# Optimization experiments

Hardware: AMD Instinct MI355X
Metric: run time of the kernel (lower is better)

The kernel has to match this reference:

```python
import jax, jax.numpy as jnp
import numpy as np

D = 1024
H = 16
HD = D // H
DFF = 4 * D
B, L = 2, 2048
EPS = 1e-5


def setup_inputs() -> dict:
    key = jax.random.key(0)
    ks = jax.random.split(key, 12)
    s = lambda fan_in: 1.0 / np.sqrt(fan_in)
    inp = {
        "x": jax.random.normal(ks[0], (B, L, D), jnp.float32),
        "mask": jnp.ones((1, 1, L, L), jnp.bool_),
        "ln_g": jnp.ones((D,), jnp.float32),
        "ln_b": jnp.zeros((D,), jnp.float32),
        "qkv_w": jax.random.uniform(ks[1], (3 * D, D), jnp.float32, -s(D), s(D)),
        "qkv_b": jax.random.uniform(ks[2], (3 * D,), jnp.float32, -s(D), s(D)),
        "wo_w": jax.random.uniform(ks[3], (D, D), jnp.float32, -s(D), s(D)),
        "wo_b": jax.random.uniform(ks[4], (D,), jnp.float32, -s(D), s(D)),
        "m0_w": jax.random.uniform(ks[5], (DFF, D), jnp.float32, -s(D), s(D)),
        "m0_b": jax.random.uniform(ks[6], (DFF,), jnp.float32, -s(D), s(D)),
        "m1_w": jax.random.uniform(ks[7], (D, DFF), jnp.float32, -s(DFF), s(DFF)),
        "m1_b": jax.random.uniform(ks[8], (D,), jnp.float32, -s(DFF), s(DFF)),
    }
    return inp


def _layer_norm(x, g, b):
    mu = jnp.mean(x, axis=-1, keepdims=True)
    var = jnp.var(x, axis=-1, keepdims=True)
    return (x - mu) * jax.lax.rsqrt(var + EPS) * g + b


def reference(x, mask, ln_g, ln_b, qkv_w, qkv_b, wo_w, wo_b, m0_w, m0_b, m1_w, m1_b):
    b, l, d = x.shape
    # --- pre-norm self-attention ---
    xn = _layer_norm(x, ln_g, ln_b)
    qkv = xn @ qkv_w.T + qkv_b                       # [B, L, 3D]
    qkv = qkv.reshape(b, l, 3, H, HD).transpose(2, 0, 3, 1, 4)  # [3, B, H, L, HD]
    q, k, v = qkv[0], qkv[1], qkv[2]
    scores = jnp.einsum("bhld,bhmd->bhlm", q, k) / np.sqrt(HD)  # [B, H, L, L]
    scores = jnp.where(mask, scores, -1e9)
    attn = jax.nn.softmax(scores, axis=-1)
    ctx = jnp.einsum("bhlm,bhmd->bhld", attn, v)     # [B, H, L, HD]
    ctx = ctx.transpose(0, 2, 1, 3).reshape(b, l, d)
    x = x + ctx @ wo_w.T + wo_b
    # --- GELU MLP (same shared LayerNorm params) ---
    xn = _layer_norm(x, ln_g, ln_b)
    h = jax.nn.gelu(xn @ m0_w.T + m0_b, approximate=False)
    return x + h @ m1_w.T + m1_b
```

## Files before the change

### kernel.cpp

```cpp
#include <hip/hip_runtime.h>
#include <hip/hip_bf16.h>
#include <math.h>

#define BL 4096
#define DM 1024
#define NH 16
#define HD 64
#define DFF 4096
#define SEQ 2048
#define EPS 1e-5f
#define QSCALE 0.18033688011112042f

typedef __bf16 bf16x8 __attribute__((ext_vector_type(8)));
typedef float f32x4 __attribute__((ext_vector_type(4)));
typedef float f32x16 __attribute__((ext_vector_type(16)));

__device__ __forceinline__ unsigned short f2bf(float f) {
    __hip_bfloat16 h = __float2bfloat16(f);
    return *reinterpret_cast<unsigned short*>(&h);
}

__device__ __forceinline__ void gload_lds16(const void* g, void* l) {
    __builtin_amdgcn_global_load_lds(
        (const __attribute__((address_space(1))) unsigned int*)g,
        (__attribute__((address_space(3))) unsigned int*)l,
        16, 0, 0);
}

__global__ __launch_bounds__(256)
void f2b4_kernel(const float* __restrict__ s0, const float* __restrict__ s1,
                 const float* __restrict__ s2, const float* __restrict__ s3,
                 unsigned short* __restrict__ d0, unsigned short* __restrict__ d1,
                 unsigned short* __restrict__ d2, unsigned short* __restrict__ d3,
                 int n0, int n1, int n2, int n3) {
    int i = blockIdx.x * 256 + threadIdx.x;
    const float* s; unsigned short* d; int j = i;
    if (j < n0) { s = s0; d = d0; }
    else if ((j -= n0) < n1) { s = s1; d = d1; }
    else if ((j -= n1) < n2) { s = s2; d = d2; }
    else if ((j -= n2) < n3) { s = s3; d = d3; }
    else return;
    float4 v = ((const float4*)s)[j];
    ushort4 o = {f2bf(v.x), f2bf(v.y), f2bf(v.z), f2bf(v.w)};
    ((ushort4*)d)[j] = o;
}

__global__ __launch_bounds__(256)
void ln_kernel(const float* __restrict__ x, const float* __restrict__ g,
               const float* __restrict__ b, unsigned short* __restrict__ o) {
    int row = blockIdx.x;
    int tid = threadIdx.x;
    const float* xr = x + (size_t)row * DM;
    float4 v = *(const float4*)(xr + tid * 4);
    float s  = v.x + v.y + v.z + v.w;
    float ss = v.x*v.x + v.y*v.y + v.z*v.z + v.w*v.w;
    #pragma unroll
    for (int off = 32; off > 0; off >>= 1) {
        s  += __shfl_down(s, off);
        ss += __shfl_down(ss, off);
    }
    __shared__ float ps[4], pss[4];
    __shared__ float sh_mu, sh_rs;
    int wid = tid >> 6, lane = tid & 63;
    if (lane == 0) { ps[wid] = s; pss[wid] = ss; }
    __syncthreads();
    if (tid == 0) {
        float S = ps[0] + ps[1] + ps[2] + ps[3];
        float SS = pss[0] + pss[1] + pss[2] + pss[3];
        float mu = S * (1.0f / DM);
        float var = SS * (1.0f / DM) - mu * mu;
        sh_mu = mu;
        sh_rs = 1.0f / sqrtf(var + EPS);
    }
    __syncthreads();
    float mu = sh_mu, rs = sh_rs;
    float4 gv = *(const float4*)(g + tid * 4);
    float4 bv = *(const float4*)(b + tid * 4);
    ushort4 ov;
    ov.x = f2bf((v.x - mu) * rs * gv.x + bv.x);
    ov.y = f2bf((v.y - mu) * rs * gv.y + bv.y);
    ov.z = f2bf((v.z - mu) * rs * gv.z + bv.z);
    ov.w = f2bf((v.w - mu) * rs * gv.w + bv.w);
    *(ushort4*)(o + (size_t)row * DM + tid * 4) = ov;
}

template <int EPI, int TN, int BK, int KSPLIT, typename OUT_T>
__global__ __launch_bounds__(256)
void gemm_bt_mfma(const unsigned short* __restrict__ A,
                  const unsigned short* __restrict__ B,
                  const float* __restrict__ bias, const float* __restrict__ res,
                  OUT_T* __restrict__ C, int M, int N, int K,
                  unsigned short* __restrict__ vt) {
    constexpr int RPC = 512 / BK;
    constexpr int CA  = 128 / RPC;
    constexpr int CB  = TN / RPC;
    constexpr int FJ  = TN / 32;
    __shared__ unsigned short As[128 * BK];
    __shared__ unsigned short Bs[TN * BK];
    const int tid = threadIdx.x, lane = tid & 63, wave = tid >> 6;

    const int id   = blockIdx.x;
    const int xcd  = id & 7, slot = id >> 3;
    const int R    = (M / 128) >> 3;
    const int by   = xcd * R + (slot % R);
    const int bx   = slot / R;
    const int m0 = by * 128, n0 = bx * TN;
    const int wm = (wave >> 1) * 64, wn = (wave & 1) * (TN / 2);
    const int k0 = blockIdx.y * (K / KSPLIT);

    const int srow = (BK == 32) ? (lane >> 2) : (lane >> 3);
    const int scol = (BK == 32) ? (lane & 3) * 8
                                : ((lane & 7) ^ (srow & 7)) * 8;
    const int fr = lane & 15;
    const int g  = lane >> 4;

    f32x4 acc[4][FJ] = {};

    for (int kt = k0; kt < k0 + K / KSPLIT; kt += BK) {
        __syncthreads();
        #pragma unroll
        for (int ci = 0; ci < (CA + CB) / 4; ci++) {
            const int c = ci * 4 + wave;
            if (c < CA)
                gload_lds16(A + (size_t)(m0 + c * RPC + srow) * K + kt + scol,
                            (char*)As + c * 1024);
            else
                gload_lds16(B + (size_t)(n0 + (c - CA) * RPC + srow) * K + kt + scol,
                            (char*)Bs + (c - CA) * 1024);
        }
        __syncthreads();

        #pragma unroll
        for (int ko = 0; ko < BK / 32; ko++) {
            const int col = (BK == 32) ? (ko * 32 + g * 8)
                                       : (((ko * 4 + g) ^ (fr & 7)) * 8);
            bf16x8 af[4], bfv[FJ];
            #pragma unroll
            for (int i = 0; i < 4; i++)
                af[i] = *(const bf16x8*)(As + (wm + i * 16 + fr) * BK + col);
            #pragma unroll
            for (int j = 0; j < FJ; j++)
                bfv[j] = *(const bf16x8*)(Bs + (wn + j * 16 + fr) * BK + col);
            #pragma unroll
            for (int i = 0; i < 4; i++)
                #pragma unroll
                for (int j = 0; j < FJ; j++)
                    acc[i][j] = __builtin_amdgcn_mfma_f32_16x16x32_bf16(af[i], bfv[j], acc[i][j], 0, 0, 0);
        }
    }

    const int col  = lane & 15;
    const int rowq = (lane >> 4) * 4;
    const bool kz0 = (KSPLIT == 1) || (blockIdx.y == 0);
    float bs[FJ];
    #pragma unroll
    for (int j = 0; j < FJ; j++) bs[j] = bias[n0 + wn + j * 16 + col];
    #pragma unroll
    for (int i = 0; i < 4; i++) {
        #pragma unroll
        for (int r = 0; r < 4; r++) {
            const size_t row = (size_t)(m0 + wm + i * 16 + rowq + r);
            #pragma unroll
            for (int j = 0; j < FJ; j++) {
                const int c = n0 + wn + j * 16 + col;
                const size_t off = row * N + c;
                float v = acc[i][j][r];
                if (EPI != 4) v += bs[j];
                if (EPI == 1) v += res[off];
                if (EPI == 2) {
                    float u = v * (0.7978845608028654f + 0.035677408136300125f * v * v);
                    float e = __builtin_amdgcn_exp2f(u * 2.885390081777927f);
                    float th = 1.0f - 2.0f * __builtin_amdgcn_rcpf(e + 1.0f);
                    v = 0.5f * v * (1.0f + th);
                }
                if (EPI == 3) {
                    if (c < 2048) {
                        float vq = (c < 1024) ? v * QSCALE : v;
                        ((unsigned short*)C)[off] = f2bf(vq);
                    } else {
                        int d = c & 63, hh = (c >> 6) & 15;
                        int bb = (int)(row >> 11), l = (int)(row & 2047);
                        vt[((size_t)((bb * 16 + hh) * 64 + d)) * 2048 + l] = f2bf(v);
                    }
                } else if (EPI == 4) {
                    if (kz0) v += bs[j];
                    unsafeAtomicAdd((float*)C + off, v);
                } else if constexpr (sizeof(OUT_T) == 2) {
                    ((unsigned short*)C)[off] = f2bf(v);
                } else {
                    ((float*)C)[off] = v;
                }
            }
        }
    }
}

__global__ __launch_bounds__(256)
void attn_mfma(const unsigned short* __restrict__ qkv,
               const unsigned short* __restrict__ vt,
               unsigned short* __restrict__ ctx) {
    __shared__ unsigned short Ks[64 * 64];
    __shared__ unsigned short Vts[64 * 64];
    const int bid = blockIdx.x;
    const int qt = bid & 15, h = (bid >> 4) & 15, b = bid >> 8;
    const int tid = threadIdx.x, lane = tid & 63, wave = tid >> 6;
    const int hh = lane >> 5, mm = lane & 31;
    const int q0 = b * 2048 + qt * 128 + wave * 32;

    bf16x8 qf[4];
    const unsigned short* qb = qkv + (size_t)(q0 + mm) * 3072 + h * 64 + hh * 8;
    #pragma unroll
    for (int s = 0; s < 4; s++) qf[s] = *(const bf16x8*)(qb + s * 16);

    const int skey = lane >> 3;
    const int sgr  = (lane & 7) ^ (skey & 7);
    const unsigned short* kbase = qkv + ((size_t)(b * 2048) + skey) * 3072 + 1024 + h * 64 + sgr * 8;
    const unsigned short* vbase = vt + ((size_t)((b * 16 + h) * 64) + skey) * 2048 + sgr * 8;

    float l_lane = 0.0f;
    f32x16 o_acc[2] = {};

    for (int kt = 0; kt < SEQ; kt += 64) {
        __syncthreads();
        #pragma unroll
        for (int rep = 0; rep < 2; rep++) {
            int c = rep * 4 + wave;
            gload_lds16(kbase + (size_t)(kt + c * 8) * 3072, (char*)Ks + c * 1024);
            gload_lds16(vbase + (size_t)(c * 8) * 2048 + kt, (char*)Vts + c * 1024);
        }
        __syncthreads();

        f32x16 sT[2] = {};
        #pragma unroll
        for (int t = 0; t < 2; t++)
            #pragma unroll
            for (int s = 0; s < 4; s++) {
                bf16x8 kf = *(const bf16x8*)(Ks + (t * 32 + mm) * 64 + ((s * 2 + hh) ^ (mm & 7)) * 8);
                sT[t] = __builtin_amdgcn_mfma_f32_32x32x16_bf16(kf, qf[s], sT[t], 0, 0, 0);
            }

        unsigned int pk[2][8];
        #pragma unroll
        for (int t = 0; t < 2; t++)
            #pragma unroll
            for (int e = 0; e < 8; e++) {
                float p0 = __builtin_amdgcn_exp2f(sT[t][2 * e]);
                float p1 = __builtin_amdgcn_exp2f(sT[t][2 * e + 1]);
                l_lane += p0 + p1;
                pk[t][e] = ((unsigned int)f2bf(p1) << 16) | f2bf(p0);
            }

        #pragma unroll
        for (int w = 0; w < 4; w++) {
            const int t = w >> 1, eb = (w & 1) * 4;
            unsigned int sx = hh ? pk[t][eb + 0] : pk[t][eb + 2];
            unsigned int sy = hh ? pk[t][eb + 1] : pk[t][eb + 3];
            unsigned int rx = (unsigned int)__shfl_xor((int)sx, 32);
            unsigned int ry = (unsigned int)__shfl_xor((int)sy, 32);
            union { unsigned int u[4]; bf16x8 v; } af;
            af.u[0] = hh ? rx : pk[t][eb + 0];
            af.u[1] = hh ? ry : pk[t][eb + 1];
            af.u[2] = hh ? pk[t][eb + 2] : rx;
            af.u[3] = hh ? pk[t][eb + 3] : ry;
            #pragma unroll
            for (int dt = 0; dt < 2; dt++) {
                bf16x8 vf = *(const bf16x8*)(Vts + (dt * 32 + mm) * 64 + ((w * 2 + hh) ^ (mm & 7)) * 8);
                o_acc[dt] = __builtin_amdgcn_mfma_f32_32x32x16_bf16(af.v, vf, o_acc[dt], 0, 0, 0);
            }
        }
    }

    float inv_own = 1.0f / (l_lane + __shfl_xor(l_lane, 32));
    #pragma unroll
    for (int r = 0; r < 16; r++) {
        const int rowq = (r & 3) + 8 * (r >> 2) + 4 * hh;
        float inv = __shfl(inv_own, rowq);
        size_t base = (size_t)(q0 + rowq) * 1024 + h * 64 + mm;
        ctx[base]      = f2bf(o_acc[0][r] * inv);
        ctx[base + 32] = f2bf(o_acc[1][r] * inv);
    }
}

extern "C" void kernel_launch(void* const* d_in, const int* in_sizes, int n_in,
                              void* d_out, int out_size, void* d_ws, size_t ws_size,
                              hipStream_t stream) {
    const float* x     = (const float*)d_in[0];
    const float* ln_g  = (const float*)d_in[2];
    const float* ln_b  = (const float*)d_in[3];
    const float* qkv_w = (const float*)d_in[4];
    const float* qkv_b = (const float*)d_in[5];
    const float* wo_w  = (const float*)d_in[6];
    const float* wo_b  = (const float*)d_in[7];
    const float* m0_w  = (const float*)d_in[8];
    const float* m0_b  = (const float*)d_in[9];
    const float* m1_w  = (const float*)d_in[10];
    const float* m1_b  = (const float*)d_in[11];
    float* out = (float*)d_out;

    char* ws = (char*)d_ws;
    unsigned short* xn_bf  = (unsigned short*)(ws);
    unsigned short* qkv_bf = (unsigned short*)(ws + (size_t)8  * 1024 * 1024);
    unsigned short* vt_bf  = (unsigned short*)(ws + (size_t)32 * 1024 * 1024);
    unsigned short* ctx_bf = (unsigned short*)(ws + (size_t)40 * 1024 * 1024);
    unsigned short* h_bf   = (unsigned short*)(ws + (size_t)48 * 1024 * 1024);
    unsigned short* qkvw_b = (unsigned short*)(ws + (size_t)80 * 1024 * 1024);
    unsigned short* wow_b  = (unsigned short*)(ws + (size_t)86 * 1024 * 1024);
    unsigned short* m0w_b  = (unsigned short*)(ws + (size_t)88 * 1024 * 1024);
    unsigned short* m1w_b  = (unsigned short*)(ws + (size_t)96 * 1024 * 1024);

    {
        int n0 = 3 * DM * DM / 4, n1 = DM * DM / 4, n2 = DFF * DM / 4, n3 = DM * DFF / 4;
        int tot = n0 + n1 + n2 + n3;
        f2b4_kernel<<<(tot + 255) / 256, 256, 0, stream>>>(
            qkv_w, wo_w, m0_w, m1_w, qkvw_b, wow_b, m0w_b, m1w_b, n0, n1, n2, n3);
    }

    ln_kernel<<<BL, 256, 0, stream>>>(x, ln_g, ln_b, xn_bf);
    gemm_bt_mfma<3, 128, 32, 1, unsigned short><<<(3072 / 128) * (BL / 128), 256, 0, stream>>>(
        xn_bf, qkvw_b, qkv_b, nullptr, qkv_bf, BL, 3072, DM, vt_bf);
    attn_mfma<<<2 * NH * (SEQ / 128), 256, 0, stream>>>(qkv_bf, vt_bf, ctx_bf);
    gemm_bt_mfma<1, 64, 32, 1, float><<<(DM / 64) * (BL / 128), 256, 0, stream>>>(
        ctx_bf, wow_b, wo_b, x, out, BL, DM, DM, nullptr);
    ln_kernel<<<BL, 256, 0, stream>>>(out, ln_g, ln_b, xn_bf);
    gemm_bt_mfma<2, 128, 32, 1, unsigned short><<<(DFF / 128) * (BL / 128), 256, 0, stream>>>(
        xn_bf, m0w_b, m0_b, nullptr, h_bf, BL, DFF, DM, nullptr);
    gemm_bt_mfma<4, 64, 64, 2, float><<<dim3((DM / 64) * (BL / 128), 2), 256, 0, stream>>>(
        h_bf, m1w_b, m1_b, nullptr, out, BL, DM, DFF, nullptr);
}
```

Before: 369.0 us.

## Give each attention wave two query groups, remap blocks per XCD, cheaper bf16 pack

The attention kernel now runs 2 waves per block, and each wave handles 64 query rows as two 32-row groups. This reuses every K and V fragment read from LDS across two MFMAs and halves the LDS traffic per query. Block indices are remapped so all query tiles of a (batch, head) pair land on the same XCD, which should improve L2 reuse of K/V. The bf16 packing of probabilities now uses a round-half-up add plus v_perm instead of two conversions, which changes rounding slightly. Register pressure roughly doubles for accumulators, which may reduce occupancy.

```diff
diff --git a/kernel.cpp b/kernel.cpp
--- a/kernel.cpp
+++ b/kernel.cpp
@@ -18,6 +18,12 @@
 __device__ __forceinline__ unsigned short f2bf(float f) {
     __hip_bfloat16 h = __float2bfloat16(f);
     return *reinterpret_cast<unsigned short*>(&h);
+}
+
+__device__ __forceinline__ unsigned int pack2bf(float p0, float p1) {
+    unsigned int u0 = __builtin_bit_cast(unsigned int, p0) + 0x8000u;
+    unsigned int u1 = __builtin_bit_cast(unsigned int, p1) + 0x8000u;
+    return __builtin_amdgcn_perm(u1, u0, 0x07060302);
 }
 
 __device__ __forceinline__ void gload_lds16(const void* g, void* l) {
@@ -195,89 +201,107 @@
     }
 }
 
-__global__ __launch_bounds__(256)
+__global__ __launch_bounds__(128)
 void attn_mfma(const unsigned short* __restrict__ qkv,
                const unsigned short* __restrict__ vt,
                unsigned short* __restrict__ ctx) {
     __shared__ unsigned short Ks[64 * 64];
     __shared__ unsigned short Vts[64 * 64];
     const int bid = blockIdx.x;
-    const int qt = bid & 15, h = (bid >> 4) & 15, b = bid >> 8;
+    const int xcd = bid & 7, sl = bid >> 3;
+    const int qt = sl & 15, pg = sl >> 4;
+    const int pair = pg * 8 + xcd;
+    const int h = pair & 15, b = pair >> 4;
     const int tid = threadIdx.x, lane = tid & 63, wave = tid >> 6;
     const int hh = lane >> 5, mm = lane & 31;
-    const int q0 = b * 2048 + qt * 128 + wave * 32;
-
-    bf16x8 qf[4];
-    const unsigned short* qb = qkv + (size_t)(q0 + mm) * 3072 + h * 64 + hh * 8;
-    #pragma unroll
-    for (int s = 0; s < 4; s++) qf[s] = *(const bf16x8*)(qb + s * 16);
+    const int qw0 = b * 2048 + qt * 128 + wave * 64;
+
+    bf16x8 qf[2][4];
+    #pragma unroll
+    for (int g2 = 0; g2 < 2; g2++) {
+        const unsigned short* qb = qkv + (size_t)(qw0 + g2 * 32 + mm) * 3072 + h * 64 + hh * 8;
+        #pragma unroll
+        for (int s = 0; s < 4; s++) qf[g2][s] = *(const bf16x8*)(qb + s * 16);
+    }
 
     const int skey = lane >> 3;
     const int sgr  = (lane & 7) ^ (skey & 7);
     const unsigned short* kbase = qkv + ((size_t)(b * 2048) + skey) * 3072 + 1024 + h * 64 + sgr * 8;
     const unsigned short* vbase = vt + ((size_t)((b * 16 + h) * 64) + skey) * 2048 + sgr * 8;
 
-    float l_lane = 0.0f;
-    f32x16 o_acc[2] = {};
+    float l_lane[2] = {};
+    f32x16 o_acc[2][2] = {};
 
     for (int kt = 0; kt < SEQ; kt += 64) {
         __syncthreads();
         #pragma unroll
-        for (int rep = 0; rep < 2; rep++) {
-            int c = rep * 4 + wave;
+        for (int rep = 0; rep < 4; rep++) {
+            int c = rep * 2 + wave;
             gload_lds16(kbase + (size_t)(kt + c * 8) * 3072, (char*)Ks + c * 1024);
             gload_lds16(vbase + (size_t)(c * 8) * 2048 + kt, (char*)Vts + c * 1024);
         }
         __syncthreads();
 
-        f32x16 sT[2] = {};
-        #pragma unroll
-        for (int t = 0; t < 2; t++)
-            #pragma unroll
-            for (int s = 0; s < 4; s++) {
-                bf16x8 kf = *(const bf16x8*)(Ks + (t * 32 + mm) * 64 + ((s * 2 + hh) ^ (mm & 7)) * 8);
-                sT[t] = __builtin_amdgcn_mfma_f32_32x32x16_bf16(kf, qf[s], sT[t], 0, 0, 0);
-            }
-
-        unsigned int pk[2][8];
-        #pragma unroll
-        for (int t = 0; t < 2; t++)
-            #pragma unroll
-            for (int e = 0; e < 8; e++) {
-                float p0 = __builtin_amdgcn_exp2f(sT[t][2 * e]);
-                float p1 = __builtin_amdgcn_exp2f(sT[t][2 * e + 1]);
-                l_lane += p0 + p1;
-                pk[t][e] = ((unsigned int)f2bf(p1) << 16) | f2bf(p0);
-            }
+        unsigned int pk[2][2][8];
+        #pragma unroll
+        for (int g2 = 0; g2 < 2; g2++) {
+            f32x16 sT[2] = {};
+            #pragma unroll
+            for (int t = 0; t < 2; t++)
+                #pragma unroll
+                for (int s = 0; s < 4; s++) {
+                    bf16x8 kf = *(const bf16x8*)(Ks + (t * 32 + mm) * 64 + ((s * 2 + hh) ^ (mm & 7)) * 8);
+                    sT[t] = __builtin_amdgcn_mfma_f32_32x32x16_bf16(kf, qf[g2][s], sT[t], 0, 0, 0);
+                }
+            #pragma unroll
+            for (int t = 0; t < 2; t++)
+                #pragma unroll
+                for (int e = 0; e < 8; e++) {
+                    float p0 = __builtin_amdgcn_exp2f(sT[t][2 * e]);
+                    float p1 = __builtin_amdgcn_exp2f(sT[t][2 * e + 1]);
+                    l_lane[g2] += p0 + p1;
+                    pk[g2][t][e] = pack2bf(p0, p1);
+                }
+        }
 
         #pragma unroll
         for (int w = 0; w < 4; w++) {
             const int t = w >> 1, eb = (w & 1) * 4;
-            unsigned int sx = hh ? pk[t][eb + 0] : pk[t][eb + 2];
-            unsigned int sy = hh ? pk[t][eb + 1] : pk[t][eb + 3];
-            unsigned int rx = (unsigned int)__shfl_xor((int)sx, 32);
-            unsigned int ry = (unsigned int)__shfl_xor((int)sy, 32);
-            union { unsigned int u[4]; bf16x8 v; } af;
-            af.u[0] = hh ? rx : pk[t][eb + 0];
-            af.u[1] = hh ? ry : pk[t][eb + 1];
-            af.u[2] = hh ? pk[t][eb + 2] : rx;
-            af.u[3] = hh ? pk[t][eb + 3] : ry;
+            bf16x8 af[2];
+            #pragma unroll
+            for (int g2 = 0; g2 < 2; g2++) {
+                unsigned int sx = hh ? pk[g2][t][eb + 0] : pk[g2][t][eb + 2];
+                unsigned int sy = hh ? pk[g2][t][eb + 1] : pk[g2][t][eb + 3];
+                unsigned int rx = (unsigned int)__shfl_xor((int)sx, 32);
+                unsigned int ry = (unsigned int)__shfl_xor((int)sy, 32);
+                union { unsigned int u[4]; bf16x8 v; } a;
+                a.u[0] = hh ? rx : pk[g2][t][eb + 0];
+                a.u[1] = hh ? ry : pk[g2][t][eb + 1];
+                a.u[2] = hh ? pk[g2][t][eb + 2] : rx;
+                a.u[3] = hh ? pk[g2][t][eb + 3] : ry;
+                af[g2] = a.v;
+            }
             #pragma unroll
             for (int dt = 0; dt < 2; dt++) {
                 bf16x8 vf = *(const bf16x8*)(Vts + (dt * 32 + mm) * 64 + ((w * 2 + hh) ^ (mm & 7)) * 8);
-                o_acc[dt] = __builtin_amdgcn_mfma_f32_32x32x16_bf16(af.v, vf, o_acc[dt], 0, 0, 0);
+                #pragma unroll
+                for (int g2 = 0; g2 < 2; g2++)
+                    o_acc[g2][dt] = __builtin_amdgcn_mfma_f32_32x32x16_bf16(af[g2], vf, o_acc[g2][dt], 0, 0, 0);
             }
         }
     }
 
-    float inv_own = 1.0f / (l_lane + __shfl_xor(l_lane, 32));
-    #pragma unroll
-    for (int r = 0; r < 16; r++) {
-        const int rowq = (r & 3) + 8 * (r >> 2) + 4 * hh;
-        float inv = __shfl(inv_own, rowq);
-        size_t base = (size_t)(q0 + rowq) * 1024 + h * 64 + mm;
-        ctx[base]      = f2bf(o_acc[0][r] * inv);
-        ctx[base + 32] = f2bf(o_acc[1][r] * inv);
+    #pragma unroll
+    for (int g2 = 0; g2 < 2; g2++) {
+        float inv_own = 1.0f / (l_lane[g2] + __shfl_xor(l_lane[g2], 32));
+        #pragma unroll
+        for (int r = 0; r < 16; r++) {
+            const int rowq = (r & 3) + 8 * (r >> 2) + 4 * hh;
+            float inv = __shfl(inv_own, rowq);
+            size_t base = (size_t)(qw0 + g2 * 32 + rowq) * 1024 + h * 64 + mm;
+            ctx[base]      = f2bf(o_acc[g2][0][r] * inv);
+            ctx[base + 32] = f2bf(o_acc[g2][1][r] * inv);
+        }
     }
 }
 
@@ -318,7 +342,7 @@
     ln_kernel<<<BL, 256, 0, stream>>>(x, ln_g, ln_b, xn_bf);
     gemm_bt_mfma<3, 128, 32, 1, unsigned short><<<(3072 / 128) * (BL / 128), 256, 0, stream>>>(
         xn_bf, qkvw_b, qkv_b, nullptr, qkv_bf, BL, 3072, DM, vt_bf);
-    attn_mfma<<<2 * NH * (SEQ / 128), 256, 0, stream>>>(qkv_bf, vt_bf, ctx_bf);
+    attn_mfma<<<2 * NH * (SEQ / 128), 128, 0, stream>>>(qkv_bf, vt_bf, ctx_bf);
     gemm_bt_mfma<1, 64, 32, 1, float><<<(DM / 64) * (BL / 128), 256, 0, stream>>>(
         ctx_bf, wow_b, wo_b, x, out, BL, DM, DM, nullptr);
     ln_kernel<<<BL, 256, 0, stream>>>(out, ln_g, ln_b, xn_bf);
```

New measurement: 372.5 us. About the same (+1.0%).
